# Kernel tuning notes

Measured on AMD Instinct MI355X. Metric: run time of the kernel, lower is better.

The kernel has to match this reference:

```python
import jax, jax.numpy as jnp
import numpy as np

B, K, H, W = 8, 1024, 24, 24
C = H * W            # in_channels = 576
NH = 6               # hardcoded num_heads
HD = C // NH         # 96


def setup_inputs() -> dict:
    key = jax.random.key(0)
    ks = jax.random.split(key, 8)
    s = 1.0 / np.sqrt(C)
    return {
        "input1": jax.random.normal(ks[0], (B, K, H, W), jnp.float32),
        "input2": jax.random.normal(ks[1], (B, K, H, W), jnp.float32),
        "Wq": jax.random.uniform(ks[2], (C, C), jnp.float32, -s, s),
        "bq": jax.random.uniform(ks[3], (C,), jnp.float32, -s, s),
        "Wk": jax.random.uniform(ks[4], (C, C), jnp.float32, -s, s),
        "bk": jax.random.uniform(ks[5], (C,), jnp.float32, -s, s),
        "Wv": jax.random.uniform(ks[6], (C, C), jnp.float32, -s, s),
        "bv": jax.random.uniform(ks[7], (C,), jnp.float32, -s, s),
    }


def reference(input1, input2, Wq, bq, Wk, bk, Wv, bv):
    b, k, h, w = input1.shape
    c = h * w
    x1 = input1.reshape(b, k, c)
    x2 = input2.reshape(b, k, c)
    # torch nn.Linear: y = x @ W^T + b
    q = x1 @ Wq.T + bq                      # [b, k, c]
    kk = x2 @ Wk.T + bk
    v = x2 @ Wv.T + bv
    # torch .view scrambles: [b, k, c] -> [b, NH, c//NH, k] (row-major reshape)
    q = q.reshape(b, NH, c // NH, k)
    kk = kk.reshape(b, NH, c // NH, k)
    v = v.reshape(b, NH, c // NH, k)
    # scores = q^T k over head-dim; NOTE: no 1/sqrt(d) scaling in original
    scores = jnp.einsum('bhdq,bhdk->bhqk', q, kk)   # [b, NH, k, k]
    weights = jax.nn.softmax(scores, axis=-1)
    # context = value @ weights^T -> [b, NH, hd, k]
    ctx = jnp.einsum('bhdk,bhqk->bhdq', v, weights)
    return ctx.reshape(b, k, h, w)
```

## Files before the change

### kernel.cpp

```cpp
#include <hip/hip_runtime.h>
#include <cmath>

#define BATCH 8
#define KDIM  1024
#define CH    576
#define NHEAD 6
#define HDIM  96

typedef _Float16 f16;
typedef f16 f16x4 __attribute__((ext_vector_type(4)));
typedef f16 f16x8 __attribute__((ext_vector_type(8)));
typedef float f32x16 __attribute__((ext_vector_type(16)));
typedef unsigned int u32;

#define PSZ  (BATCH * KDIM * CH)
#define WSZ  (CH * CH)

__device__ inline f32x16 zero16() {
    f32x16 z;
#pragma unroll
    for (int r = 0; r < 16; ++r) z[r] = 0.f;
    return z;
}

__global__ __launch_bounds__(256) void convert_w2(
    const float* __restrict__ Wq, const float* __restrict__ Wk,
    const float* __restrict__ Wv, f16* __restrict__ wh)
{
    const int k0 = blockIdx.x;
    const int xb = blockIdx.y;
    const int z  = blockIdx.z;
    const float* src = (z == 0) ? Wq : (z == 1) ? Wk : Wv;
    const int tid = threadIdx.x;

    __shared__ f16 Ws2[192 * 88];

#pragma unroll
    for (int r = 0; r < 12; ++r) {
        int idx = r * 256 + tid;
        int row = idx >> 4, c4 = idx & 15;
        float4 u = *(const float4*)&src[(size_t)(xb * 192 + row) * CH + k0 * 64 + c4 * 4];
        f16x4 hv;
        hv[0] = (f16)u.x; hv[1] = (f16)u.y; hv[2] = (f16)u.z; hv[3] = (f16)u.w;
        *(f16x4*)&Ws2[row * 88 + c4 * 4] = hv;
    }
    __syncthreads();

    f16* dst = wh + ((size_t)((z * 3 + xb) * 9 + k0) * 24) * 512;
#pragma unroll
    for (int rr = 0; rr < 6; ++rr) {
        int cc = rr * 256 + tid;
        int lc = cc >> 6, lane = cc & 63;
        int ks = lc / 6, rem = lc % 6;
        int hw = rem / 3, nt = rem % 3;
        int n_local = hw * 96 + nt * 32 + (lane & 31);
        int kk = ks * 16 + (lane >> 5) * 8;
        f16x8 v = *(const f16x8*)&Ws2[n_local * 88 + kk];
        *(f16x8*)&dst[(size_t)cc * 8] = v;
    }
}

__global__ __launch_bounds__(256, 2) void proj_kernel(
    const float* __restrict__ x1, const float* __restrict__ x2,
    const f16* __restrict__ wh,
    const float* __restrict__ bq, const float* __restrict__ bk,
    const float* __restrict__ bv,
    f16* __restrict__ qf, f16* __restrict__ kf, f16* __restrict__ vf)
{
    const int bid = blockIdx.x;
    const int k8  = bid & 7;
    const int j   = bid >> 3;
    const int xb  = j % 3;
    const int z   = (j / 3) % 3;
    const int y   = k8 + 8 * (j / 9);

    const float* A    = (z == 0) ? x1 : x2;
    const float* bias = (z == 0) ? bq : (z == 1) ? bk : bv;
    f16* dst          = (z == 0) ? qf : (z == 1) ? kf : vf;

    __shared__ f16 As[128 * 72];

    const int tid = threadIdx.x;
    const int lane = tid & 63, w = tid >> 6;
    const int l31 = lane & 31, half = lane >> 5;
    const int mw = 64 * (w & 1), nh = 96 * (w >> 1);
    const int nBase = xb * 192;
    const int mBase = y * 128;

    int arow[4], ach[4];
#pragma unroll
    for (int r = 0; r < 4; ++r) {
        int idx = r * 256 + tid;
        arow[r] = idx >> 3; ach[r] = idx & 7;
    }

    const f16* Wfrag = wh + ((size_t)(z * 3 + xb) * 216 + (size_t)(w >> 1) * 3) * 512
                          + (size_t)lane * 8;

    float4 aP[4][2];
#pragma unroll
    for (int r = 0; r < 4; ++r) {
        const float* p = &A[(size_t)(mBase + arow[r]) * CH + ach[r] * 8];
        aP[r][0] = ((const float4*)p)[0];
        aP[r][1] = ((const float4*)p)[1];
    }

    f16x8 wc[12];
#pragma unroll
    for (int ks = 0; ks < 4; ++ks)
#pragma unroll
        for (int nt = 0; nt < 3; ++nt)
            wc[ks * 3 + nt] = *(const f16x8*)&Wfrag[(size_t)(ks * 6 + nt) * 512];

    f32x16 acc[2][3] = {{zero16(), zero16(), zero16()},
                        {zero16(), zero16(), zero16()}};

    for (int k0i = 0; k0i < 9; ++k0i) {
        __syncthreads();
#pragma unroll
        for (int r = 0; r < 4; ++r) {
            f16x8 hv;
            hv[0] = (f16)aP[r][0].x; hv[1] = (f16)aP[r][0].y;
            hv[2] = (f16)aP[r][0].z; hv[3] = (f16)aP[r][0].w;
            hv[4] = (f16)aP[r][1].x; hv[5] = (f16)aP[r][1].y;
            hv[6] = (f16)aP[r][1].z; hv[7] = (f16)aP[r][1].w;
            *(f16x8*)&As[arow[r] * 72 + ach[r] * 8] = hv;
        }
        __syncthreads();
        if (k0i + 1 < 9) {
#pragma unroll
            for (int r = 0; r < 4; ++r) {
                const float* p = &A[(size_t)(mBase + arow[r]) * CH + (k0i + 1) * 64 + ach[r] * 8];
                aP[r][0] = ((const float4*)p)[0];
                aP[r][1] = ((const float4*)p)[1];
            }
        }
#pragma unroll
        for (int ks = 0; ks < 4; ++ks) {
            f16x8 a0 = *(const f16x8*)&As[(mw + l31) * 72 + 16 * ks + 8 * half];
            f16x8 a1 = *(const f16x8*)&As[(mw + 32 + l31) * 72 + 16 * ks + 8 * half];
#pragma unroll
            for (int nt = 0; nt < 3; ++nt) {
                acc[0][nt] = __builtin_amdgcn_mfma_f32_32x32x16_f16(a0, wc[ks * 3 + nt], acc[0][nt], 0, 0, 0);
                acc[1][nt] = __builtin_amdgcn_mfma_f32_32x32x16_f16(a1, wc[ks * 3 + nt], acc[1][nt], 0, 0, 0);
            }
        }
        if (k0i + 1 < 9) {
            const f16* Wn = Wfrag + (size_t)(k0i + 1) * 24 * 512;
#pragma unroll
            for (int ks = 0; ks < 4; ++ks)
#pragma unroll
                for (int nt = 0; nt < 3; ++nt)
                    wc[ks * 3 + nt] = *(const f16x8*)&Wn[(size_t)(ks * 6 + nt) * 512];
        }
    }

#pragma unroll
    for (int nt = 0; nt < 3; ++nt) {
        int n = nBase + nh + 32 * nt + l31;
        float bsv = bias[n];
#pragma unroll
        for (int ms = 0; ms < 2; ++ms)
#pragma unroll
            for (int r = 0; r < 16; ++r) {
                int m = mBase + mw + 32 * ms + (r & 3) + 8 * (r >> 2) + 4 * half;
                dst[(size_t)m * CH + n] = (f16)(acc[ms][nt][r] + bsv);
            }
    }
}

__global__ __launch_bounds__(256) void repack_qkv(
    const f16* __restrict__ qf, const f16* __restrict__ kf,
    const f16* __restrict__ vf,
    f16* __restrict__ QF, f16* __restrict__ KF, f16* __restrict__ VF)
{
    const int tt = blockIdx.x;
    const int bh = blockIdx.y;
    const int z  = blockIdx.z;
    const int tid = threadIdx.x;

    if (z < 2) {
        const f16* src = z ? kf : qf;
        f16* dst = z ? KF : QF;

        __shared__ f16 Ts[96 * 72];
        const int rowbase = (bh / NHEAD) * CH + (bh % NHEAD) * HDIM;

#pragma unroll
        for (int r = 0; r < 3; ++r) {
            int idx = r * 256 + tid;
            int d = idx >> 3, g = idx & 7;
            *(f16x8*)&Ts[d * 72 + g * 8] =
                *(const f16x8*)&src[(size_t)(rowbase + d) * KDIM + tt * 64 + g * 8];
        }
        __syncthreads();

        f16* dblk = dst + ((size_t)bh * 16 + tt) * 6144;
#pragma unroll
        for (int r = 0; r < 3; ++r) {
            int c = r * 256 + tid;
            int lane = c & 63;
            int ks = (c >> 6) % 6;
            int jg = c / 384;
            int l31 = lane & 31, half = lane >> 5;
            int jl = jg * 32 + l31;
            int d0 = ks * 16 + half * 8;
            f16x8 v;
#pragma unroll
            for (int u = 0; u < 8; ++u) v[u] = Ts[(d0 + u) * 72 + jl];
            *(f16x8*)&dblk[(size_t)c * 8] = v;
        }
    } else {
        const f16* vbase = vf + ((size_t)(bh / NHEAD) * CH + (bh % NHEAD) * HDIM) * KDIM;
        f16* dblk = VF + ((size_t)bh * 16 + tt) * 6144;

#pragma unroll
        for (int r = 0; r < 3; ++r) {
            int c = r * 256 + tid;
            int lane = c & 63;
            int t  = (c >> 6) % 3;
            int kq = ((c >> 6) / 3) & 1;
            int jg = c / 384;
            int l31 = lane & 31, half = lane >> 5;
            int d = t * 32 + l31;
            int j = tt * 64 + jg * 32 + kq * 16 + half * 8;
            f16x8 v = *(const f16x8*)&vbase[(size_t)d * KDIM + j];
            *(f16x8*)&dblk[(size_t)c * 8] = v;
        }
    }
}

__global__ __launch_bounds__(256, 3) void attn_kernel(
    const f16* __restrict__ QF, const f16* __restrict__ KF,
    const f16* __restrict__ VF, float* __restrict__ out)
{
    __shared__ __align__(16) char smem[25600];

    const int bh = blockIdx.x;
    const int qt = blockIdx.y;
    const int h  = bh % NHEAD;
    const int b  = bh / NHEAD;

    const int tid = threadIdx.x;
    const int lane = tid & 63, w = tid >> 6;
    const int ih = w & 1, jg = w >> 1;
    const int l31 = lane & 31, half = lane >> 5;
    const int iw = 32 * ih;

    const f16* Qblk  = QF + ((size_t)bh * 16 + qt) * 6144 + (size_t)ih * 3072 + (size_t)lane * 8;
    const f16* Kfrag = KF + (size_t)bh * 16 * 6144 + (size_t)jg * 3072 + (size_t)lane * 8;
    const f16* Vfrag = VF + (size_t)bh * 16 * 6144 + (size_t)jg * 3072 + (size_t)lane * 8;

    f16x8 qfr[6];
#pragma unroll
    for (int ks = 0; ks < 6; ++ks) {
        qfr[ks] = *(const f16x8*)&Qblk[ks * 512];
#pragma unroll
        for (int u = 0; u < 8; ++u)
            qfr[ks][u] = (f16)((float)qfr[ks][u] * 1.44269504f);
    }

    f16x8 kc[6], vc[6];
#pragma unroll
    for (int ks = 0; ks < 6; ++ks)
        kc[ks] = *(const f16x8*)&Kfrag[ks * 512];
#pragma unroll
    for (int kq = 0; kq < 2; ++kq)
#pragma unroll
        for (int t = 0; t < 3; ++t)
            vc[kq * 3 + t] = *(const f16x8*)&Vfrag[kq * 1536 + t * 512];

    float l_run = 0.f;
    f32x16 Oacc[3] = {zero16(), zero16(), zero16()};

    for (int jt = 0; jt < 16; ++jt) {
        f32x16 s0 = zero16();
#pragma unroll
        for (int ks = 0; ks < 6; ++ks)
            s0 = __builtin_amdgcn_mfma_f32_32x32x16_f16(kc[ks], qfr[ks], s0, 0, 0, 0);

        if (jt + 1 < 16) {
            const f16* Kt = Kfrag + (size_t)(jt + 1) * 6144;
#pragma unroll
            for (int ks = 0; ks < 6; ++ks)
                kc[ks] = *(const f16x8*)&Kt[ks * 512];
        }

        f16x4 pq[4];
#pragma unroll
        for (int r = 0; r < 16; ++r) {
            float e = __builtin_amdgcn_exp2f(s0[r] - 26.0f);
            l_run += e;
            pq[r >> 2][r & 3] = (f16)e;
        }

#pragma unroll
        for (int kq = 0; kq < 2; ++kq) {
            union { f16x4 h; u32 u[2]; } snd, rcv, keep;
            keep.h = half ? pq[2 * kq + 1] : pq[2 * kq];
            snd.h  = half ? pq[2 * kq]     : pq[2 * kq + 1];
            rcv.u[0] = __shfl_xor((int)snd.u[0], 32);
            rcv.u[1] = __shfl_xor((int)snd.u[1], 32);
            f16x8 bp;
            if (half == 0) {
#pragma unroll
                for (int v = 0; v < 4; ++v) { bp[v] = keep.h[v]; bp[4 + v] = rcv.h[v]; }
            } else {
#pragma unroll
                for (int v = 0; v < 4; ++v) { bp[v] = rcv.h[v]; bp[4 + v] = keep.h[v]; }
            }
#pragma unroll
            for (int t = 0; t < 3; ++t)
                Oacc[t] = __builtin_amdgcn_mfma_f32_32x32x16_f16(vc[kq * 3 + t], bp, Oacc[t], 0, 0, 0);
        }

        if (jt + 1 < 16) {
            const f16* Vt = Vfrag + (size_t)(jt + 1) * 6144;
#pragma unroll
            for (int kq = 0; kq < 2; ++kq)
#pragma unroll
                for (int t = 0; t < 3; ++t)
                    vc[kq * 3 + t] = *(const f16x8*)&Vt[kq * 1536 + t * 512];
        }
    }

    l_run += __shfl_xor(l_run, 32);

    float* Oscr = (float*)smem;
    float* lScr = (float*)(smem + 25344);
    if (jg == 1) {
        if (half == 0) lScr[iw + l31] = l_run;
        float* od = Oscr + ih * 3168;
#pragma unroll
        for (int t = 0; t < 3; ++t)
#pragma unroll
            for (int r = 0; r < 16; ++r) {
                int d = 32 * t + (r & 3) + 8 * (r >> 2) + 4 * half;
                od[d * 33 + l31] = Oacc[t][r];
            }
    }
    __syncthreads();
    if (jg == 0) {
        float linv = 1.0f / (l_run + lScr[iw + l31]);
        const float* od = Oscr + ih * 3168;
        float* obase = out + ((size_t)b * CH + (size_t)h * HDIM) * KDIM
                           + qt * 64 + iw + l31;
#pragma unroll
        for (int t = 0; t < 3; ++t)
#pragma unroll
            for (int r = 0; r < 16; ++r) {
                int d = 32 * t + (r & 3) + 8 * (r >> 2) + 4 * half;
                obase[(size_t)d * KDIM] =
                    (Oacc[t][r] + od[d * 33 + l31]) * linv;
            }
    }
}

extern "C" void kernel_launch(void* const* d_in, const int* in_sizes, int n_in,
                              void* d_out, int out_size, void* d_ws, size_t ws_size,
                              hipStream_t stream)
{
    const float* x1 = (const float*)d_in[0];
    const float* x2 = (const float*)d_in[1];
    const float* Wq = (const float*)d_in[2];
    const float* bq = (const float*)d_in[3];
    const float* Wk = (const float*)d_in[4];
    const float* bk = (const float*)d_in[5];
    const float* Wv = (const float*)d_in[6];
    const float* bv = (const float*)d_in[7];
    float* out = (float*)d_out;

    const size_t P = PSZ;
    f16* qf = (f16*)d_ws;
    f16* kf = qf + P;
    f16* vf = kf + P;
    f16* QF = vf + P;
    f16* KF = QF + P;
    f16* VF = KF + P;
    f16* wh = VF + P;

    dim3 wgrid(9, 3, 3);
    convert_w2<<<wgrid, 256, 0, stream>>>(Wq, Wk, Wv, wh);

    proj_kernel<<<576, 256, 0, stream>>>(x1, x2, wh, bq, bk, bv, qf, kf, vf);

    dim3 rgrid(KDIM / 64, BATCH * NHEAD, 3);
    repack_qkv<<<rgrid, 256, 0, stream>>>(qf, kf, vf, QF, KF, VF);

    dim3 agrid(BATCH * NHEAD, KDIM / 64);
    attn_kernel<<<agrid, 256, 0, stream>>>(QF, KF, VF, out);
}
```

Baseline: 167.0 us.

## Pre-convert inputs to fp16 and write V directly in attention layout

```diff
diff --git a/kernel.cpp b/kernel.cpp
--- a/kernel.cpp
+++ b/kernel.cpp
@@ -23,49 +23,71 @@
     return z;
 }
 
-__global__ __launch_bounds__(256) void convert_w2(
+__global__ __launch_bounds__(256) void convert_all(
+    const float* __restrict__ x1, const float* __restrict__ x2,
     const float* __restrict__ Wq, const float* __restrict__ Wk,
-    const float* __restrict__ Wv, f16* __restrict__ wh)
+    const float* __restrict__ Wv,
+    f16* __restrict__ x1h, f16* __restrict__ x2h, f16* __restrict__ wh)
 {
-    const int k0 = blockIdx.x;
-    const int xb = blockIdx.y;
-    const int z  = blockIdx.z;
-    const float* src = (z == 0) ? Wq : (z == 1) ? Wk : Wv;
+    const int bid = blockIdx.x;
     const int tid = threadIdx.x;
 
     __shared__ f16 Ws2[192 * 88];
 
-#pragma unroll
-    for (int r = 0; r < 12; ++r) {
-        int idx = r * 256 + tid;
-        int row = idx >> 4, c4 = idx & 15;
-        float4 u = *(const float4*)&src[(size_t)(xb * 192 + row) * CH + k0 * 64 + c4 * 4];
-        f16x4 hv;
-        hv[0] = (f16)u.x; hv[1] = (f16)u.y; hv[2] = (f16)u.z; hv[3] = (f16)u.w;
-        *(f16x4*)&Ws2[row * 88 + c4 * 4] = hv;
-    }
-    __syncthreads();
-
-    f16* dst = wh + ((size_t)((z * 3 + xb) * 9 + k0) * 24) * 512;
-#pragma unroll
-    for (int rr = 0; rr < 6; ++rr) {
-        int cc = rr * 256 + tid;
-        int lc = cc >> 6, lane = cc & 63;
-        int ks = lc / 6, rem = lc % 6;
-        int hw = rem / 3, nt = rem % 3;
-        int n_local = hw * 96 + nt * 32 + (lane & 31);
-        int kk = ks * 16 + (lane >> 5) * 8;
-        f16x8 v = *(const f16x8*)&Ws2[n_local * 88 + kk];
-        *(f16x8*)&dst[(size_t)cc * 8] = v;
+    if (bid < 81) {
+        const int z  = bid / 27;
+        const int xb = (bid % 27) / 9;
+        const int k0 = bid % 9;
+        const float* src = (z == 0) ? Wq : (z == 1) ? Wk : Wv;
+
+#pragma unroll
+        for (int r = 0; r < 12; ++r) {
+            int idx = r * 256 + tid;
+            int row = idx >> 4, c4 = idx & 15;
+            float4 u = *(const float4*)&src[(size_t)(xb * 192 + row) * CH + k0 * 64 + c4 * 4];
+            f16x4 hv;
+            hv[0] = (f16)u.x; hv[1] = (f16)u.y; hv[2] = (f16)u.z; hv[3] = (f16)u.w;
+            *(f16x4*)&Ws2[row * 88 + c4 * 4] = hv;
+        }
+        __syncthreads();
+
+        f16* dst = wh + ((size_t)((z * 3 + xb) * 9 + k0) * 24) * 512;
+#pragma unroll
+        for (int rr = 0; rr < 6; ++rr) {
+            int cc = rr * 256 + tid;
+            int lc = cc >> 6, lane = cc & 63;
+            int ks = lc / 6, rem = lc % 6;
+            int hw = rem / 3, nt = rem % 3;
+            int n_local = hw * 96 + nt * 32 + (lane & 31);
+            int kk = ks * 16 + (lane >> 5) * 8;
+            f16x8 v = *(const f16x8*)&Ws2[n_local * 88 + kk];
+            *(f16x8*)&dst[(size_t)cc * 8] = v;
+        }
+    } else {
+        int idx = (bid - 81) * 256 + tid;
+        const float* src;
+        f16* dst;
+        if (idx < PSZ / 8) { src = x1; dst = x1h; }
+        else {
+            idx -= PSZ / 8;
+            if (idx >= PSZ / 8) return;
+            src = x2; dst = x2h;
+        }
+        float4 u0 = ((const float4*)src)[2 * idx];
+        float4 u1 = ((const float4*)src)[2 * idx + 1];
+        f16x8 hv;
+        hv[0] = (f16)u0.x; hv[1] = (f16)u0.y; hv[2] = (f16)u0.z; hv[3] = (f16)u0.w;
+        hv[4] = (f16)u1.x; hv[5] = (f16)u1.y; hv[6] = (f16)u1.z; hv[7] = (f16)u1.w;
+        ((f16x8*)dst)[idx] = hv;
     }
 }
 
 __global__ __launch_bounds__(256, 2) void proj_kernel(
-    const float* __restrict__ x1, const float* __restrict__ x2,
+    const f16* __restrict__ x1h, const f16* __restrict__ x2h,
     const f16* __restrict__ wh,
     const float* __restrict__ bq, const float* __restrict__ bk,
     const float* __restrict__ bv,
-    f16* __restrict__ qf, f16* __restrict__ kf, f16* __restrict__ vf)
+    f16* __restrict__ qf, f16* __restrict__ kf, f16* __restrict__ VF)
 {
     const int bid = blockIdx.x;
     const int k8  = bid & 7;
@@ -74,11 +96,12 @@
     const int z   = (j / 3) % 3;
     const int y   = k8 + 8 * (j / 9);
 
-    const float* A    = (z == 0) ? x1 : x2;
+    const f16* A      = (z == 0) ? x1h : x2h;
     const float* bias = (z == 0) ? bq : (z == 1) ? bk : bv;
-    f16* dst          = (z == 0) ? qf : (z == 1) ? kf : vf;
-
-    __shared__ f16 As[128 * 72];
+
+    __shared__ __align__(16) char sm[25600];
+    f16* As = (f16*)sm;
+    f16* Es = (f16*)sm;
 
     const int tid = threadIdx.x;
     const int lane = tid & 63, w = tid >> 6;
@@ -97,13 +120,10 @@
     const f16* Wfrag = wh + ((size_t)(z * 3 + xb) * 216 + (size_t)(w >> 1) * 3) * 512
                           + (size_t)lane * 8;
 
-    float4 aP[4][2];
-#pragma unroll
-    for (int r = 0; r < 4; ++r) {
-        const float* p = &A[(size_t)(mBase + arow[r]) * CH + ach[r] * 8];
-        aP[r][0] = ((const float4*)p)[0];
-        aP[r][1] = ((const float4*)p)[1];
-    }
+    f16x8 aP[4];
+#pragma unroll
+    for (int r = 0; r < 4; ++r)
+        aP[r] = *(const f16x8*)&A[(size_t)(mBase + arow[r]) * CH + ach[r] * 8];
 
     f16x8 wc[12];
 #pragma unroll
@@ -118,22 +138,13 @@
     for (int k0i = 0; k0i < 9; ++k0i) {
         __syncthreads();
 #pragma unroll
-        for (int r = 0; r < 4; ++r) {
-            f16x8 hv;
-            hv[0] = (f16)aP[r][0].x; hv[1] = (f16)aP[r][0].y;
-            hv[2] = (f16)aP[r][0].z; hv[3] = (f16)aP[r][0].w;
-            hv[4] = (f16)aP[r][1].x; hv[5] = (f16)aP[r][1].y;
-            hv[6] = (f16)aP[r][1].z; hv[7] = (f16)aP[r][1].w;
-            *(f16x8*)&As[arow[r] * 72 + ach[r] * 8] = hv;
-        }
+        for (int r = 0; r < 4; ++r)
+            *(f16x8*)&As[arow[r] * 72 + ach[r] * 8] = aP[r];
         __syncthreads();
         if (k0i + 1 < 9) {
 #pragma unroll
-            for (int r = 0; r < 4; ++r) {
-                const float* p = &A[(size_t)(mBase + arow[r]) * CH + (k0i + 1) * 64 + ach[r] * 8];
-                aP[r][0] = ((const float4*)p)[0];
-                aP[r][1] = ((const float4*)p)[1];
-            }
+            for (int r = 0; r < 4; ++r)
+                aP[r] = *(const f16x8*)&A[(size_t)(mBase + arow[r]) * CH + (k0i + 1) * 64 + ach[r] * 8];
         }
 #pragma unroll
         for (int ks = 0; ks < 4; ++ks) {
@@ -155,78 +166,95 @@
         }
     }
 
-#pragma unroll
-    for (int nt = 0; nt < 3; ++nt) {
-        int n = nBase + nh + 32 * nt + l31;
-        float bsv = bias[n];
-#pragma unroll
-        for (int ms = 0; ms < 2; ++ms)
-#pragma unroll
-            for (int r = 0; r < 16; ++r) {
-                int m = mBase + mw + 32 * ms + (r & 3) + 8 * (r >> 2) + 4 * half;
-                dst[(size_t)m * CH + n] = (f16)(acc[ms][nt][r] + bsv);
-            }
-    }
-}
-
-__global__ __launch_bounds__(256) void repack_qkv(
+    if (z < 2) {
+        f16* dst = (z == 0) ? qf : kf;
+#pragma unroll
+        for (int nt = 0; nt < 3; ++nt) {
+            int n = nBase + nh + 32 * nt + l31;
+            float bsv = bias[n];
+#pragma unroll
+            for (int ms = 0; ms < 2; ++ms)
+#pragma unroll
+                for (int r = 0; r < 16; ++r) {
+                    int m = mBase + mw + 32 * ms + (r & 3) + 8 * (r >> 2) + 4 * half;
+                    dst[(size_t)m * CH + n] = (f16)(acc[ms][nt][r] + bsv);
+                }
+        }
+    } else {
+        const int b      = y >> 3;
+        const int kkBase = (y & 7) * 128;
+#pragma unroll
+        for (int hs = 0; hs < 2; ++hs) {
+            __syncthreads();
+            if ((w & 1) == hs) {
+#pragma unroll
+                for (int nt = 0; nt < 3; ++nt) {
+                    int nloc = nh + 32 * nt + l31;
+                    float bsv = bias[nBase + nloc];
+#pragma unroll
+                    for (int ms = 0; ms < 2; ++ms)
+#pragma unroll
+                        for (int r = 0; r < 16; ++r) {
+                            int row_l = 32 * ms + (r & 3) + 8 * (r >> 2) + 4 * half;
+                            Es[row_l * 200 + nloc] = (f16)(acc[ms][nt][r] + bsv);
+                        }
+                }
+            }
+            __syncthreads();
+#pragma unroll
+            for (int rr = 0; rr < 6; ++rr) {
+                int o = rr * 256 + tid;
+                int row_l = o / 24, sl = o % 24;
+                int f = (kkBase + hs * 64 + row_l) * 576 + nBase + sl * 8;
+                int h = f / 98304;
+                int rem = f - h * 98304;
+                int d = rem >> 10, t = rem & 1023;
+                int tt2 = t >> 6, tl = t & 63;
+                int c = (tl >> 5) * 384 + ((tl >> 4) & 1) * 192
+                      + (d >> 5) * 64 + (d & 31) + 32 * ((tl >> 3) & 1);
+                f16x8 v = *(const f16x8*)&Es[row_l * 200 + sl * 8];
+                *(f16x8*)&VF[((size_t)((b * NHEAD + h) * 16 + tt2)) * 6144 + (size_t)c * 8] = v;
+            }
+        }
+    }
+}
+
+__global__ __launch_bounds__(256) void repack_qk(
     const f16* __restrict__ qf, const f16* __restrict__ kf,
-    const f16* __restrict__ vf,
-    f16* __restrict__ QF, f16* __restrict__ KF, f16* __restrict__ VF)
+    f16* __restrict__ QF, f16* __restrict__ KF)
 {
     const int tt = blockIdx.x;
     const int bh = blockIdx.y;
-    const int z  = blockIdx.z;
+    const f16* src = blockIdx.z ? kf : qf;
+    f16* dst = blockIdx.z ? KF : QF;
     const int tid = threadIdx.x;
 
-    if (z < 2) {
-        const f16* src = z ? kf : qf;
-        f16* dst = z ? KF : QF;
-
-        __shared__ f16 Ts[96 * 72];
-        const int rowbase = (bh / NHEAD) * CH + (bh % NHEAD) * HDIM;
-
-#pragma unroll
-        for (int r = 0; r < 3; ++r) {
-            int idx = r * 256 + tid;
-            int d = idx >> 3, g = idx & 7;
-            *(f16x8*)&Ts[d * 72 + g * 8] =
-                *(const f16x8*)&src[(size_t)(rowbase + d) * KDIM + tt * 64 + g * 8];
-        }
-        __syncthreads();
-
-        f16* dblk = dst + ((size_t)bh * 16 + tt) * 6144;
-#pragma unroll
-        for (int r = 0; r < 3; ++r) {
-            int c = r * 256 + tid;
-            int lane = c & 63;
-            int ks = (c >> 6) % 6;
-            int jg = c / 384;
-            int l31 = lane & 31, half = lane >> 5;
-            int jl = jg * 32 + l31;
-            int d0 = ks * 16 + half * 8;
-            f16x8 v;
-#pragma unroll
-            for (int u = 0; u < 8; ++u) v[u] = Ts[(d0 + u) * 72 + jl];
-            *(f16x8*)&dblk[(size_t)c * 8] = v;
-        }
-    } else {
-        const f16* vbase = vf + ((size_t)(bh / NHEAD) * CH + (bh % NHEAD) * HDIM) * KDIM;
-        f16* dblk = VF + ((size_t)bh * 16 + tt) * 6144;
-
-#pragma unroll
-        for (int r = 0; r < 3; ++r) {
-            int c = r * 256 + tid;
-            int lane = c & 63;
-            int t  = (c >> 6) % 3;
-            int kq = ((c >> 6) / 3) & 1;
-            int jg = c / 384;
-            int l31 = lane & 31, half = lane >> 5;
-            int d = t * 32 + l31;
-            int j = tt * 64 + jg * 32 + kq * 16 + half * 8;
-            f16x8 v = *(const f16x8*)&vbase[(size_t)d * KDIM + j];
-            *(f16x8*)&dblk[(size_t)c * 8] = v;
-        }
+    __shared__ f16 Ts[96 * 72];
+    const int rowbase = (bh / NHEAD) * CH + (bh % NHEAD) * HDIM;
+
+#pragma unroll
+    for (int r = 0; r < 3; ++r) {
+        int idx = r * 256 + tid;
+        int d = idx >> 3, g = idx & 7;
+        *(f16x8*)&Ts[d * 72 + g * 8] =
+            *(const f16x8*)&src[(size_t)(rowbase + d) * KDIM + tt * 64 + g * 8];
+    }
+    __syncthreads();
+
+    f16* dblk = dst + ((size_t)bh * 16 + tt) * 6144;
+#pragma unroll
+    for (int r = 0; r < 3; ++r) {
+        int c = r * 256 + tid;
+        int lane = c & 63;
+        int ks = (c >> 6) % 6;
+        int jg = c / 384;
+        int l31 = lane & 31, half = lane >> 5;
+        int jl = jg * 32 + l31;
+        int d0 = ks * 16 + half * 8;
+        f16x8 v;
+#pragma unroll
+        for (int u = 0; u < 8; ++u) v[u] = Ts[(d0 + u) * 72 + jl];
+        *(f16x8*)&dblk[(size_t)c * 8] = v;
     }
 }
 
@@ -371,21 +399,22 @@
     float* out = (float*)d_out;
 
     const size_t P = PSZ;
-    f16* qf = (f16*)d_ws;
-    f16* kf = qf + P;
-    f16* vf = kf + P;
-    f16* QF = vf + P;
-    f16* KF = QF + P;
-    f16* VF = KF + P;
-    f16* wh = VF + P;
-
-    dim3 wgrid(9, 3, 3);
-    convert_w2<<<wgrid, 256, 0, stream>>>(Wq, Wk, Wv, wh);
-
-    proj_kernel<<<576, 256, 0, stream>>>(x1, x2, wh, bq, bk, bv, qf, kf, vf);
-
-    dim3 rgrid(KDIM / 64, BATCH * NHEAD, 3);
-    repack_qkv<<<rgrid, 256, 0, stream>>>(qf, kf, vf, QF, KF, VF);
+    f16* x1h = (f16*)d_ws;
+    f16* x2h = x1h + P;
+    f16* qf  = x2h + P;
+    f16* kf  = qf + P;
+    f16* QF  = kf + P;
+    f16* KF  = QF + P;
+    f16* VF  = KF + P;
+    f16* wh  = VF + P;
+
+    const int xblocks = 2 * (PSZ / 8) / 256;
+    convert_all<<<81 + xblocks, 256, 0, stream>>>(x1, x2, Wq, Wk, Wv, x1h, x2h, wh);
+
+    proj_kernel<<<576, 256, 0, stream>>>(x1h, x2h, wh, bq, bk, bv, qf, kf, VF);
+
+    dim3 rgrid(KDIM / 64, BATCH * NHEAD, 2);
+    repack_qk<<<rgrid, 256, 0, stream>>>(qf, kf, QF, KF);
 
     dim3 agrid(BATCH * NHEAD, KDIM / 64);
     attn_kernel<<<agrid, 256, 0, stream>>>(QF, KF, VF, out);
```

Result: faster. 160.0 us (-4.2%).
